# Optimization experiments

Hardware: AMD Instinct MI355X
Metric: run time of the kernel (lower is better)

The kernel has to match this reference:

```python
import jax, jax.numpy as jnp
import numpy as np

N_EMBD = 1024
N_HEAD = 16
HEAD_DIM = N_EMBD // N_HEAD


def setup_inputs() -> dict:
    key = jax.random.key(0)
    ks = jax.random.split(key, 9)
    B, T, C = 4, 2048, N_EMBD
    s = 1.0 / np.sqrt(C)
    return {
        "x": jax.random.normal(ks[0], (B, T, C), dtype=jnp.float32),
        "Wq": jax.random.normal(ks[1], (C, C), dtype=jnp.float32) * s,
        "bq": jnp.zeros((C,), dtype=jnp.float32),
        "Wk": jax.random.normal(ks[2], (C, C), dtype=jnp.float32) * s,
        "bk": jnp.zeros((C,), dtype=jnp.float32),
        "Wv": jax.random.normal(ks[3], (C, C), dtype=jnp.float32) * s,
        "bv": jnp.zeros((C,), dtype=jnp.float32),
        "Wo": jax.random.normal(ks[4], (C, C), dtype=jnp.float32) * s,
        "bo": jnp.zeros((C,), dtype=jnp.float32),
    }


def reference(x, Wq, bq, Wk, bk, Wv, bv, Wo, bo):
    B, T, C = x.shape
    H, D = N_HEAD, HEAD_DIM
    # torch Linear: y = x @ W.T + b ; here W stored as (in, out) so y = x @ W + b
    q = (x @ Wq + bq).reshape(B, T, H, D).transpose(0, 2, 1, 3)  # [B,H,T,D]
    k = (x @ Wk + bk).reshape(B, T, H, D).transpose(0, 2, 1, 3)
    v = (x @ Wv + bv).reshape(B, T, H, D).transpose(0, 2, 1, 3)
    scores = jnp.einsum('bhqd,bhkd->bhqk', q, k) / jnp.sqrt(jnp.float32(D))
    causal = jnp.tril(jnp.ones((T, T), dtype=bool))  # [T,T]
    scores = jnp.where(causal[None, None, :, :], scores, -jnp.inf)
    weights = jax.nn.softmax(scores, axis=-1)
    # dropout disabled (eval mode / deterministic reference)
    out = jnp.einsum('bhqk,bhkd->bhqd', weights, v)  # [B,H,T,D]
    out = out.transpose(0, 2, 1, 3).reshape(B, T, C)
    return out @ Wo + bo
```

## Files before the change

### kernel.cpp

```cpp
#include <hip/hip_runtime.h>
#include <stdint.h>
#include <stddef.h>

#define NB 4
#define NT 2048
#define NC 1024
#define NH 16
#define ND 64
#define NM (NB*NT)

typedef __bf16 bf16_t;
typedef __attribute__((ext_vector_type(8)))  __bf16 bf16x8;
typedef __attribute__((ext_vector_type(4)))  __bf16 bf16x4;
typedef __attribute__((ext_vector_type(2)))  __bf16 bf16x2;
typedef __attribute__((ext_vector_type(4)))  float  f32x4;
typedef __attribute__((ext_vector_type(16))) float  f32x16;
typedef __attribute__((ext_vector_type(4)))  unsigned int u32x4;

#define QK_SCALE_LOG2E 0.18033688011112042f

__device__ __forceinline__ f32x4 mfma_bf16(bf16x8 a, bf16x8 b, f32x4 c) {
  return __builtin_amdgcn_mfma_f32_16x16x32_bf16(a, b, c, 0, 0, 0);
}
__device__ __forceinline__ f32x16 mfma32(bf16x8 a, bf16x8 b, f32x16 c) {
  return __builtin_amdgcn_mfma_f32_32x32x16_bf16(a, b, c, 0, 0, 0);
}

__device__ __forceinline__ void gld_lds16(const void* g, void* l) {
  __builtin_amdgcn_global_load_lds(
      (const __attribute__((address_space(1))) void*)g,
      (__attribute__((address_space(3))) void*)l, 16, 0, 0);
}

__device__ __forceinline__ unsigned int pack_bf16(float a, float b) {
  bf16x2 t; t[0] = (bf16_t)a; t[1] = (bf16_t)b;
  return __builtin_bit_cast(unsigned int, t);
}

#if __has_builtin(__builtin_amdgcn_permlane32_swap)
typedef __attribute__((ext_vector_type(2))) unsigned int u32x2;
__device__ __forceinline__ void plswap(unsigned int &a, unsigned int &b) {
  u32x2 r = __builtin_amdgcn_permlane32_swap(a, b, false, false);
  a = r[0]; b = r[1];
}
#else
__device__ __forceinline__ void plswap(unsigned int &a, unsigned int &b) {
  asm volatile("s_nop 1\n\tv_permlane32_swap_b32 %0, %1\n\ts_nop 1"
               : "+v"(a), "+v"(b));
}
#endif

__global__ __launch_bounds__(256) void prep_kernel(
    const float* __restrict__ x, const float* __restrict__ Wq,
    const float* __restrict__ Wk, const float* __restrict__ Wv,
    const float* __restrict__ Wo,
    bf16_t* __restrict__ xb, bf16_t* __restrict__ Tq, bf16_t* __restrict__ Tk,
    bf16_t* __restrict__ Tv, bf16_t* __restrict__ To) {
  __shared__ float tile[32][33];
  if (blockIdx.x < 4096) {
    const int wsel = blockIdx.x >> 10;
    const float* W = (wsel == 0) ? Wq : (wsel == 1) ? Wk : (wsel == 2) ? Wv : Wo;
    bf16_t*     WT = (wsel == 0) ? Tq : (wsel == 1) ? Tk : (wsel == 2) ? Tv : To;
    const int blk = blockIdx.x & 1023;
    const int t = threadIdx.x;
    const int tx = t & 31, ty = t >> 5;
    const int k0 = (blk & 31) << 5;
    const int n0 = (blk >> 5) << 5;
#pragma unroll
    for (int i = 0; i < 4; ++i)
      tile[ty + 8*i][tx] = W[(size_t)(k0 + ty + 8*i)*NC + n0 + tx];
    __syncthreads();
#pragma unroll
    for (int i = 0; i < 4; ++i)
      WT[(size_t)(n0 + ty + 8*i)*NC + k0 + tx] = (bf16_t)tile[tx][ty + 8*i];
  } else {
    const int n4 = NM*NC/4;
    const int stride = 2048 * 256;
    for (int i = (blockIdx.x - 4096) * 256 + threadIdx.x; i < n4; i += stride) {
      float4 v = reinterpret_cast<const float4*>(x)[i];
      bf16x4 o;
      o[0] = (bf16_t)v.x; o[1] = (bf16_t)v.y; o[2] = (bf16_t)v.z; o[3] = (bf16_t)v.w;
      reinterpret_cast<bf16x4*>(xb)[i] = o;
    }
  }
}

template<int MODE>
__global__ __launch_bounds__(512, 2) void gemm_bt256_kernel(
    const bf16_t* __restrict__ A, const bf16_t* __restrict__ BT,
    int M, int N, int K,
    bf16_t* __restrict__ qo, bf16_t* __restrict__ ko, bf16_t* __restrict__ vo,
    const float* __restrict__ b0, const float* __restrict__ b1, const float* __restrict__ b2,
    float* __restrict__ outp, const float* __restrict__ bo)
{
  const int tid  = threadIdx.x;
  const int lane = tid & 63;
  const int wv   = tid >> 6;
  const int wr   = wv >> 1, wc = wv & 1;
  const int l15  = lane & 15, lg = lane >> 4;

  const int nbn = N >> 7;
  const int cpx = gridDim.x >> 3;
  const int swz = (blockIdx.x & 7)*cpx + (blockIdx.x >> 3);
  const int bm = swz / nbn, bn = swz % nbn;
  const int m0 = bm << 8, n0 = bn << 7;

  __shared__ char smem[98304];

  f32x4 acc[4][4] = {};

  int offa[4], offb[2];
#pragma unroll
  for (int p = 0; p < 4; ++p) {
    const int c = p*512 + tid;
    const int row = c >> 3, ch = (c & 7) ^ (row & 7);
    offa[p] = row*K + (ch << 3);
  }
#pragma unroll
  for (int p = 0; p < 2; ++p) {
    const int c = p*512 + tid;
    const int row = c >> 3, ch = (c & 7) ^ (row & 7);
    offb[p] = row*K + (ch << 3);
  }
  const int sega = wv << 10;

  const bf16_t* Ab = A  + (size_t)m0 * K;
  const bf16_t* Bb = BT + (size_t)n0 * K;

  const int nkt = K >> 6;

  {
    char* const As = smem;
    char* const Bs = smem + 32768;
#pragma unroll
    for (int p = 0; p < 4; ++p) gld_lds16(Ab + offa[p], As + p*8192 + sega);
#pragma unroll
    for (int p = 0; p < 2; ++p) gld_lds16(Bb + offb[p], Bs + p*8192 + sega);
  }

  for (int kt = 0; kt < nkt; ++kt) {
    char* const As = smem + (kt & 1)*49152;
    char* const Bs = As + 32768;

    asm volatile("s_waitcnt vmcnt(0)" ::: "memory");
    __builtin_amdgcn_s_barrier();
    __builtin_amdgcn_sched_barrier(0);

    if (kt + 1 < nkt) {
      char* const An = smem + ((kt + 1) & 1)*49152;
      char* const Bn = An + 32768;
      const int k0 = (kt + 1) << 6;
#pragma unroll
      for (int p = 0; p < 4; ++p) gld_lds16(Ab + k0 + offa[p], An + p*8192 + sega);
#pragma unroll
      for (int p = 0; p < 2; ++p) gld_lds16(Bb + k0 + offb[p], Bn + p*8192 + sega);
      __builtin_amdgcn_sched_barrier(0);
    }

#pragma unroll
    for (int ks = 0; ks < 2; ++ks) {
      bf16x8 af[4], bfr[4];
#pragma unroll
      for (int fr = 0; fr < 4; ++fr) {
        const int row = wr*64 + fr*16 + l15;
        const int ch  = (ks*4 + lg) ^ (row & 7);
        af[fr] = *reinterpret_cast<const bf16x8*>(As + row*128 + ch*16);
      }
#pragma unroll
      for (int fc = 0; fc < 4; ++fc) {
        const int row = wc*64 + fc*16 + l15;
        const int ch  = (ks*4 + lg) ^ (row & 7);
        bfr[fc] = *reinterpret_cast<const bf16x8*>(Bs + row*128 + ch*16);
      }
      __builtin_amdgcn_s_setprio(1);
#pragma unroll
      for (int fr = 0; fr < 4; ++fr)
#pragma unroll
        for (int fc = 0; fc < 4; ++fc)
          acc[fr][fc] = mfma_bf16(af[fr], bfr[fc], acc[fr][fc]);
      __builtin_amdgcn_s_setprio(0);
    }
  }

  if (MODE == 0 && n0 >= 2*NC) {
    bf16_t* vbuf = (bf16_t*)smem;
    const int VSTR = 264;
    __syncthreads();
#pragma unroll
    for (int fr = 0; fr < 4; ++fr) {
#pragma unroll
      for (int fc = 0; fc < 4; ++fc) {
        const int zl = wc*64 + fc*16 + l15;
        const int tl = wr*64 + fr*16 + (lg << 2);
        const float bias = b2[(n0 - 2*NC) + zl];
        bf16x4 ov;
#pragma unroll
        for (int r = 0; r < 4; ++r) ov[r] = (bf16_t)(acc[fr][fc][r] + bias);
        *reinterpret_cast<bf16x4*>(&vbuf[zl*VSTR + tl]) = ov;
      }
    }
    __syncthreads();
    const int zl  = tid >> 2;
    const int t0l = (tid & 3) << 6;
    const int zg  = (n0 - 2*NC) + zl;
    const int h   = zg >> 6, d = zg & 63;
    const int bbv = m0 >> 11;
    bf16_t* dst = vo + ((((size_t)bbv*NH + h)*ND + d)*NT) + (m0 & (NT-1)) + t0l;
#pragma unroll
    for (int u = 0; u < 8; ++u)
      *reinterpret_cast<bf16x8*>(dst + u*8) =
          *reinterpret_cast<const bf16x8*>(&vbuf[zl*VSTR + t0l + u*8]);
  } else {
#pragma unroll
    for (int fr = 0; fr < 4; ++fr) {
#pragma unroll
      for (int fc = 0; fc < 4; ++fc) {
        const int mrow0 = m0 + wr*64 + fr*16 + (lg << 2);
        const int ncol  = n0 + wc*64 + fc*16 + l15;
        if (MODE == 0) {
          const int mat = ncol >> 10, c = ncol & 1023;
          const int h = c >> 6, d = c & 63;
          bf16_t* dst = (mat == 0) ? qo : ko;
          const float* bptr = (mat == 0) ? b0 : b1;
          const float bias = bptr[c];
          const float scl = (mat == 0) ? QK_SCALE_LOG2E : 1.0f;
#pragma unroll
          for (int r = 0; r < 4; ++r) {
            const int mm = mrow0 + r;
            const int bb = mm >> 11, tt = mm & (NT - 1);
            dst[((((size_t)bb*NH + h)*NT + tt) << 6) + d] =
                (bf16_t)((acc[fr][fc][r] + bias) * scl);
          }
        } else {
          const float bias = bo[ncol];
#pragma unroll
          for (int r = 0; r < 4; ++r)
            outp[(size_t)(mrow0 + r)*N + ncol] = acc[fr][fc][r] + bias;
        }
      }
    }
  }
}

__global__ __launch_bounds__(256, 2) void attn_kernel(
    const bf16_t* __restrict__ q, const bf16_t* __restrict__ k, const bf16_t* __restrict__ vt,
    bf16_t* __restrict__ o)
{
  const int tid  = threadIdx.x;
  const int lane = tid & 63;
  const int wv   = tid >> 6;
  const int l31  = lane & 31, h = lane >> 5;

  const int tpair = blockIdx.x >> 6;
  const int bh    = blockIdx.x & 63;
  const int bb = bh >> 4, hh = bh & 15;

  __shared__ char smem[65536];
  char* const ks0 = smem;
  char* const ks1 = smem + 16384;
  char* const vs0 = smem + 32768;
  char* const vs1 = smem + 49152;

  const size_t base = (size_t)bh * (NT * ND);
  const bf16_t* Kg = k  + base;
  const bf16_t* Vg = vt + base;

  int offk[4], offv[4], segb[4];
#pragma unroll
  for (int p = 0; p < 4; ++p) {
    const int c = p*256 + tid;
    const int krow = c >> 3;
    const int kch  = (c & 7) ^ (krow & 7);
    offk[p] = krow*ND + (kch << 3);
    const int vrow = c >> 4;
    const int vdc  = (c & 15) ^ (vrow & 15);
    offv[p] = vrow*NT + (vdc << 3);
    segb[p] = (p*4 + wv) << 10;
  }

  bf16x8 ones8;
#pragma unroll
  for (int jj2 = 0; jj2 < 8; ++jj2) ones8[jj2] = (bf16_t)1.0f;

#pragma unroll
  for (int p = 0; p < 4; ++p) {
    gld_lds16(Kg + offk[p], ks0 + segb[p]);
    gld_lds16(Vg + offv[p], vs0 + segb[p]);
  }

  int jj = 0;

#pragma unroll 1
  for (int pass = 0; pass < 2; ++pass) {
    const int tile = (pass == 0) ? tpair : 15 - tpair;
    const int q0   = tile << 7;
    const int q0w  = q0 + wv*32;
    const int qg   = q0w + l31;

    bf16x8 qf[4];
    {
      const bf16_t* Qg = q + base + (size_t)qg*ND + 8*h;
#pragma unroll
      for (int ds = 0; ds < 4; ++ds)
        qf[ds] = *reinterpret_cast<const bf16x8*>(Qg + 16*ds);
    }

    f32x16 oc[2] = {};
    f32x16 lacc = {};

    const int nkv = tile + 1;

#pragma unroll 1
    for (int j = 0; j < nkv; ++j, ++jj) {
      const bool cur1 = (jj & 1) != 0;
      char* const Kc = cur1 ? ks1 : ks0;
      char* const Vc = cur1 ? vs1 : vs0;

      asm volatile("s_waitcnt vmcnt(0)" ::: "memory");
      __builtin_amdgcn_s_barrier();
      __builtin_amdgcn_sched_barrier(0);

      int nj = (j + 1 < nkv) ? (j + 1) : ((pass == 0) ? 0 : -1);
      if (nj >= 0) {
        char* const Kn = cur1 ? ks0 : ks1;
        char* const Vn = cur1 ? vs0 : vs1;
        const bf16_t* kp = Kg + (size_t)nj*(128*ND);
        const bf16_t* vp = Vg + (size_t)nj*128;
#pragma unroll
        for (int p = 0; p < 4; ++p) {
          gld_lds16(kp + offk[p], Kn + segb[p]);
          gld_lds16(vp + offv[p], Vn + segb[p]);
        }
        __builtin_amdgcn_sched_barrier(0);
      }

      const int ktile0 = j << 7;
#pragma unroll 1
      for (int hf = 0; hf < 2; ++hf) {
        const int kb0 = ktile0 + (hf << 6);
        if (kb0 > q0w + 31) break;

        f32x16 st[2] = {};
        __builtin_amdgcn_s_setprio(1);
#pragma unroll
        for (int ds = 0; ds < 4; ++ds) {
#pragma unroll
          for (int kt = 0; kt < 2; ++kt) {
            const int row = (hf*2 + kt)*32 + l31;
            const int cl  = (2*ds + h) ^ (row & 7);
            const bf16x8 kfr = *reinterpret_cast<const bf16x8*>(Kc + row*128 + cl*16);
            st[kt] = mfma32(kfr, qf[ds], st[kt]);
          }
        }
        __builtin_amdgcn_s_setprio(0);

        if (kb0 + 63 > q0w) {
          const int qrel = qg - kb0 - 4*h;
#pragma unroll
          for (int kt = 0; kt < 2; ++kt)
#pragma unroll
            for (int r = 0; r < 16; ++r) {
              const int kc = (r & 3) + 8*(r >> 2) + 32*kt;
              st[kt][r] = (kc > qrel) ? 0.0f : exp2f(st[kt][r]);
            }
        } else {
#pragma unroll
          for (int kt = 0; kt < 2; ++kt)
#pragma unroll
            for (int r = 0; r < 16; ++r)
              st[kt][r] = exp2f(st[kt][r]);
        }

#pragma unroll
        for (int kt = 0; kt < 2; ++kt) {
#pragma unroll
          for (int g = 0; g < 2; ++g) {
            unsigned int wa = pack_bf16(st[kt][8*g + 0], st[kt][8*g + 1]);
            unsigned int wb = pack_bf16(st[kt][8*g + 2], st[kt][8*g + 3]);
            unsigned int wc = pack_bf16(st[kt][8*g + 4], st[kt][8*g + 5]);
            unsigned int wd = pack_bf16(st[kt][8*g + 6], st[kt][8*g + 7]);
            plswap(wa, wc);
            plswap(wb, wd);
            u32x4 pb; pb[0] = wa; pb[1] = wb; pb[2] = wc; pb[3] = wd;
            const bf16x8 pf = __builtin_bit_cast(bf16x8, pb);
            const int cv = 2*(4*hf + 2*kt + g) + h;
            __builtin_amdgcn_s_setprio(1);
            lacc = mfma32(ones8, pf, lacc);
#pragma unroll
            for (int da = 0; da < 2; ++da) {
              const int row = 32*da + l31;
              const int lcv = cv ^ (row & 15);
              const bf16x8 vf = *reinterpret_cast<const bf16x8*>(Vc + row*256 + lcv*16);
              oc[da] = mfma32(vf, pf, oc[da]);
            }
            __builtin_amdgcn_s_setprio(0);
          }
        }
      }
    }

    const float rl = 1.0f / lacc[0];
    bf16_t* orow = o + ((size_t)bb*NT + qg)*NC + hh*ND;
#pragma unroll
    for (int da = 0; da < 2; ++da) {
#pragma unroll
      for (int u = 0; u < 4; ++u) {
        bf16x4 ov;
#pragma unroll
        for (int jj3 = 0; jj3 < 4; ++jj3) ov[jj3] = (bf16_t)(oc[da][4*u + jj3] * rl);
        *reinterpret_cast<bf16x4*>(orow + 32*da + 8*u + 4*h) = ov;
      }
    }
  }
}

extern "C" void kernel_launch(void* const* d_in, const int* in_sizes, int n_in,
                              void* d_out, int out_size, void* d_ws, size_t ws_size,
                              hipStream_t stream) {
  (void)in_sizes; (void)n_in; (void)out_size;
  const float* x  = (const float*)d_in[0];
  const float* Wq = (const float*)d_in[1];
  const float* bq = (const float*)d_in[2];
  const float* Wk = (const float*)d_in[3];
  const float* bk = (const float*)d_in[4];
  const float* Wv = (const float*)d_in[5];
  const float* bv = (const float*)d_in[6];
  const float* Wo = (const float*)d_in[7];
  const float* bo = (const float*)d_in[8];
  float* out = (float*)d_out;

  const size_t off_xb    = 0;
  const size_t off_wqkvT = 16777216;
  const size_t off_woT   = 23068672;
  const size_t off_q     = 25165824;
  const size_t off_k     = 41943040;
  const size_t off_v     = 58720256;
  const size_t off_attn  = 75497472;
  const size_t need      = 92274688;
  if (ws_size < need) return;

  char* ws = (char*)d_ws;
  bf16_t* xb    = (bf16_t*)(ws + off_xb);
  bf16_t* wqkvT = (bf16_t*)(ws + off_wqkvT);
  bf16_t* woT   = (bf16_t*)(ws + off_woT);
  bf16_t* qb    = (bf16_t*)(ws + off_q);
  bf16_t* kb    = (bf16_t*)(ws + off_k);
  bf16_t* vtb   = (bf16_t*)(ws + off_v);
  bf16_t* attnb = (bf16_t*)(ws + off_attn);

  prep_kernel<<<dim3(6144), dim3(256), 0, stream>>>(
      x, Wq, Wk, Wv, Wo, xb, wqkvT, wqkvT + 1048576, wqkvT + 2097152, woT);

  gemm_bt256_kernel<0><<<dim3(768), dim3(512), 0, stream>>>(
      xb, wqkvT, NM, 3*NC, NC, qb, kb, vtb, bq, bk, bv, nullptr, nullptr);

  attn_kernel<<<dim3(8*64), dim3(256), 0, stream>>>(qb, kb, vtb, attnb);

  gemm_bt256_kernel<1><<<dim3(256), dim3(512), 0, stream>>>(
      attnb, woT, NM, NC, NC, nullptr, nullptr, nullptr, nullptr, nullptr, nullptr,
      out, bo);
}
```

Baseline: 161.3 us.

## Process paired causal query tiles in one KV sweep sharing K/V loads

The attention kernel used to handle its two paired query tiles (tpair and 15-tpair) in sequence, walking the K/V tiles twice. It now keeps both tiles' Q fragments and accumulators live at once and walks the KV tiles a single time up to the longer tile, feeding the shorter tile only for the first nkvA steps. This halves global-to-LDS traffic for the shared prefix and cuts the number of barriers. The cost is roughly doubled accumulator and Q register state, which may raise VGPR pressure and reduce occupancy under launch_bounds(256,2).

```diff
diff --git a/kernel.cpp b/kernel.cpp
--- a/kernel.cpp
+++ b/kernel.cpp
@@ -255,6 +255,11 @@
   const int bh    = blockIdx.x & 63;
   const int bb = bh >> 4, hh = bh & 15;
 
+  const int tileA = tpair;
+  const int tileB = 15 - tpair;
+  const int nkvA  = tileA + 1;
+  const int nkvB  = tileB + 1;
+
   __shared__ char smem[65536];
   char* const ks0 = smem;
   char* const ks1 = smem + 16384;
@@ -280,7 +285,7 @@
 
   bf16x8 ones8;
 #pragma unroll
-  for (int jj2 = 0; jj2 < 8; ++jj2) ones8[jj2] = (bf16_t)1.0f;
+  for (int i = 0; i < 8; ++i) ones8[i] = (bf16_t)1.0f;
 
 #pragma unroll
   for (int p = 0; p < 4; ++p) {
@@ -288,129 +293,143 @@
     gld_lds16(Vg + offv[p], vs0 + segb[p]);
   }
 
-  int jj = 0;
-
+  const int q0wA = (tileA << 7) + wv*32, qgA = q0wA + l31;
+  const int q0wB = (tileB << 7) + wv*32, qgB = q0wB + l31;
+
+  bf16x8 qfA[4], qfB[4];
+  {
+    const bf16_t* QgA = q + base + (size_t)qgA*ND + 8*h;
+    const bf16_t* QgB = q + base + (size_t)qgB*ND + 8*h;
+#pragma unroll
+    for (int ds = 0; ds < 4; ++ds) {
+      qfA[ds] = *reinterpret_cast<const bf16x8*>(QgA + 16*ds);
+      qfB[ds] = *reinterpret_cast<const bf16x8*>(QgB + 16*ds);
+    }
+  }
+
+  f32x16 ocA[2] = {}, ocB[2] = {};
+  f32x16 laccA = {}, laccB = {};
+
+  auto chain = [&](int j, int q0w, int qg, bf16x8 (&qf)[4],
+                   f32x16 (&oc)[2], f32x16 &lacc, char* Kc, char* Vc) {
+    const int ktile0 = j << 7;
 #pragma unroll 1
-  for (int pass = 0; pass < 2; ++pass) {
-    const int tile = (pass == 0) ? tpair : 15 - tpair;
-    const int q0   = tile << 7;
-    const int q0w  = q0 + wv*32;
-    const int qg   = q0w + l31;
-
-    bf16x8 qf[4];
-    {
-      const bf16_t* Qg = q + base + (size_t)qg*ND + 8*h;
-#pragma unroll
-      for (int ds = 0; ds < 4; ++ds)
-        qf[ds] = *reinterpret_cast<const bf16x8*>(Qg + 16*ds);
-    }
-
-    f32x16 oc[2] = {};
-    f32x16 lacc = {};
-
-    const int nkv = tile + 1;
+    for (int hf = 0; hf < 2; ++hf) {
+      const int kb0 = ktile0 + (hf << 6);
+      if (kb0 > q0w + 31) break;
+
+      f32x16 st[2] = {};
+      __builtin_amdgcn_s_setprio(1);
+#pragma unroll
+      for (int ds = 0; ds < 4; ++ds) {
+#pragma unroll
+        for (int kt = 0; kt < 2; ++kt) {
+          const int row = (hf*2 + kt)*32 + l31;
+          const int cl  = (2*ds + h) ^ (row & 7);
+          const bf16x8 kfr = *reinterpret_cast<const bf16x8*>(Kc + row*128 + cl*16);
+          st[kt] = mfma32(kfr, qf[ds], st[kt]);
+        }
+      }
+      __builtin_amdgcn_s_setprio(0);
+
+      if (kb0 + 63 > q0w) {
+        const int qrel = qg - kb0 - 4*h;
+#pragma unroll
+        for (int kt = 0; kt < 2; ++kt)
+#pragma unroll
+          for (int r = 0; r < 16; ++r) {
+            const int kc = (r & 3) + 8*(r >> 2) + 32*kt;
+            st[kt][r] = (kc > qrel) ? 0.0f : exp2f(st[kt][r]);
+          }
+      } else {
+#pragma unroll
+        for (int kt = 0; kt < 2; ++kt)
+#pragma unroll
+          for (int r = 0; r < 16; ++r)
+            st[kt][r] = exp2f(st[kt][r]);
+      }
+
+#pragma unroll
+      for (int kt = 0; kt < 2; ++kt) {
+#pragma unroll
+        for (int g = 0; g < 2; ++g) {
+          unsigned int wa = pack_bf16(st[kt][8*g + 0], st[kt][8*g + 1]);
+          unsigned int wb = pack_bf16(st[kt][8*g + 2], st[kt][8*g + 3]);
+          unsigned int wc = pack_bf16(st[kt][8*g + 4], st[kt][8*g + 5]);
+          unsigned int wd = pack_bf16(st[kt][8*g + 6], st[kt][8*g + 7]);
+          plswap(wa, wc);
+          plswap(wb, wd);
+          u32x4 pb; pb[0] = wa; pb[1] = wb; pb[2] = wc; pb[3] = wd;
+          const bf16x8 pf = __builtin_bit_cast(bf16x8, pb);
+          const int cv = 2*(4*hf + 2*kt + g) + h;
+          __builtin_amdgcn_s_setprio(1);
+          lacc = mfma32(ones8, pf, lacc);
+#pragma unroll
+          for (int da = 0; da < 2; ++da) {
+            const int row = 32*da + l31;
+            const int lcv = cv ^ (row & 15);
+            const bf16x8 vf = *reinterpret_cast<const bf16x8*>(Vc + row*256 + lcv*16);
+            oc[da] = mfma32(vf, pf, oc[da]);
+          }
+          __builtin_amdgcn_s_setprio(0);
+        }
+      }
+    }
+  };
 
 #pragma unroll 1
-    for (int j = 0; j < nkv; ++j, ++jj) {
-      const bool cur1 = (jj & 1) != 0;
-      char* const Kc = cur1 ? ks1 : ks0;
-      char* const Vc = cur1 ? vs1 : vs0;
-
-      asm volatile("s_waitcnt vmcnt(0)" ::: "memory");
-      __builtin_amdgcn_s_barrier();
+  for (int j = 0; j < nkvB; ++j) {
+    const bool cur1 = (j & 1) != 0;
+    char* const Kc = cur1 ? ks1 : ks0;
+    char* const Vc = cur1 ? vs1 : vs0;
+
+    asm volatile("s_waitcnt vmcnt(0)" ::: "memory");
+    __builtin_amdgcn_s_barrier();
+    __builtin_amdgcn_sched_barrier(0);
+
+    if (j + 1 < nkvB) {
+      char* const Kn = cur1 ? ks0 : ks1;
+      char* const Vn = cur1 ? vs0 : vs1;
+      const bf16_t* kp = Kg + (size_t)(j + 1)*(128*ND);
+      const bf16_t* vp = Vg + (size_t)(j + 1)*128;
+#pragma unroll
+      for (int p = 0; p < 4; ++p) {
+        gld_lds16(kp + offk[p], Kn + segb[p]);
+        gld_lds16(vp + offv[p], Vn + segb[p]);
+      }
       __builtin_amdgcn_sched_barrier(0);
-
-      int nj = (j + 1 < nkv) ? (j + 1) : ((pass == 0) ? 0 : -1);
-      if (nj >= 0) {
-        char* const Kn = cur1 ? ks0 : ks1;
-        char* const Vn = cur1 ? vs0 : vs1;
-        const bf16_t* kp = Kg + (size_t)nj*(128*ND);
-        const bf16_t* vp = Vg + (size_t)nj*128;
-#pragma unroll
-        for (int p = 0; p < 4; ++p) {
-          gld_lds16(kp + offk[p], Kn + segb[p]);
-          gld_lds16(vp + offv[p], Vn + segb[p]);
-        }
-        __builtin_amdgcn_sched_barrier(0);
-      }
-
-      const int ktile0 = j << 7;
-#pragma unroll 1
-      for (int hf = 0; hf < 2; ++hf) {
-        const int kb0 = ktile0 + (hf << 6);
-        if (kb0 > q0w + 31) break;
-
-        f32x16 st[2] = {};
-        __builtin_amdgcn_s_setprio(1);
-#pragma unroll
-        for (int ds = 0; ds < 4; ++ds) {
-#pragma unroll
-          for (int kt = 0; kt < 2; ++kt) {
-            const int row = (hf*2 + kt)*32 + l31;
-            const int cl  = (2*ds + h) ^ (row & 7);
-            const bf16x8 kfr = *reinterpret_cast<const bf16x8*>(Kc + row*128 + cl*16);
-            st[kt] = mfma32(kfr, qf[ds], st[kt]);
-          }
-        }
-        __builtin_amdgcn_s_setprio(0);
-
-        if (kb0 + 63 > q0w) {
-          const int qrel = qg - kb0 - 4*h;
-#pragma unroll
-          for (int kt = 0; kt < 2; ++kt)
-#pragma unroll
-            for (int r = 0; r < 16; ++r) {
-              const int kc = (r & 3) + 8*(r >> 2) + 32*kt;
-              st[kt][r] = (kc > qrel) ? 0.0f : exp2f(st[kt][r]);
-            }
-        } else {
-#pragma unroll
-          for (int kt = 0; kt < 2; ++kt)
-#pragma unroll
-            for (int r = 0; r < 16; ++r)
-              st[kt][r] = exp2f(st[kt][r]);
-        }
-
-#pragma unroll
-        for (int kt = 0; kt < 2; ++kt) {
-#pragma unroll
-          for (int g = 0; g < 2; ++g) {
-            unsigned int wa = pack_bf16(st[kt][8*g + 0], st[kt][8*g + 1]);
-            unsigned int wb = pack_bf16(st[kt][8*g + 2], st[kt][8*g + 3]);
-            unsigned int wc = pack_bf16(st[kt][8*g + 4], st[kt][8*g + 5]);
-            unsigned int wd = pack_bf16(st[kt][8*g + 6], st[kt][8*g + 7]);
-            plswap(wa, wc);
-            plswap(wb, wd);
-            u32x4 pb; pb[0] = wa; pb[1] = wb; pb[2] = wc; pb[3] = wd;
-            const bf16x8 pf = __builtin_bit_cast(bf16x8, pb);
-            const int cv = 2*(4*hf + 2*kt + g) + h;
-            __builtin_amdgcn_s_setprio(1);
-            lacc = mfma32(ones8, pf, lacc);
-#pragma unroll
-            for (int da = 0; da < 2; ++da) {
-              const int row = 32*da + l31;
-              const int lcv = cv ^ (row & 15);
-              const bf16x8 vf = *reinterpret_cast<const bf16x8*>(Vc + row*256 + lcv*16);
-              oc[da] = mfma32(vf, pf, oc[da]);
-            }
-            __builtin_amdgcn_s_setprio(0);
-          }
-        }
-      }
-    }
-
-    const float rl = 1.0f / lacc[0];
-    bf16_t* orow = o + ((size_t)bb*NT + qg)*NC + hh*ND;
-#pragma unroll
-    for (int da = 0; da < 2; ++da) {
+    }
+
+    if (j < nkvA)
+      chain(j, q0wA, qgA, qfA, ocA, laccA, Kc, Vc);
+    chain(j, q0wB, qgB, qfB, ocB, laccB, Kc, Vc);
+  }
+
+  {
+    const float rl = 1.0f / laccA[0];
+    bf16_t* orow = o + ((size_t)bb*NT + qgA)*NC + hh*ND;
+#pragma unroll
+    for (int da = 0; da < 2; ++da)
 #pragma unroll
       for (int u = 0; u < 4; ++u) {
         bf16x4 ov;
 #pragma unroll
-        for (int jj3 = 0; jj3 < 4; ++jj3) ov[jj3] = (bf16_t)(oc[da][4*u + jj3] * rl);
+        for (int i = 0; i < 4; ++i) ov[i] = (bf16_t)(ocA[da][4*u + i] * rl);
         *reinterpret_cast<bf16x4*>(orow + 32*da + 8*u + 4*h) = ov;
       }
-    }
+  }
+  {
+    const float rl = 1.0f / laccB[0];
+    bf16_t* orow = o + ((size_t)bb*NT + qgB)*NC + hh*ND;
+#pragma unroll
+    for (int da = 0; da < 2; ++da)
+#pragma unroll
+      for (int u = 0; u < 4; ++u) {
+        bf16x4 ov;
+#pragma unroll
+        for (int i = 0; i < 4; ++i) ov[i] = (bf16_t)(ocB[da][4*u + i] * rl);
+        *reinterpret_cast<bf16x4*>(orow + 32*da + 8*u + 4*h) = ov;
+      }
   }
 }
 
```

Result: no change. 163.0 us (+1.0%).
